# Performance work log

Hardware: AMD Instinct MI355X
Metric: run time of the kernel (lower is better)

## Reference

```python
import jax, jax.numpy as jnp
import numpy as np

N = 100000
E = 1600000
F_IN = 512
H1, C1 = 8, 8      # layer-1: 8 heads, 8 dims each (concat -> 64)
H2, C2 = 1, 16     # layer-2: 1 head, num_classes=16
SLOPE = 0.2        # GATConv leaky_relu negative slope


def setup_inputs() -> dict:
    key = jax.random.key(0)
    ks = jax.random.split(key, 10)
    x = jax.random.normal(ks[0], (N, F_IN), dtype=jnp.float32)
    edge_index = jax.random.randint(ks[1], (2, E), 0, N, dtype=jnp.int32)
    s = 0.05
    W1 = jax.random.normal(ks[2], (F_IN, H1 * C1), dtype=jnp.float32) * s
    a1_src = jax.random.normal(ks[3], (H1, C1), dtype=jnp.float32) * s
    a1_dst = jax.random.normal(ks[4], (H1, C1), dtype=jnp.float32) * s
    b1 = jnp.zeros((H1 * C1,), dtype=jnp.float32)
    W2 = jax.random.normal(ks[5], (H1 * C1, H2 * C2), dtype=jnp.float32) * s
    a2_src = jax.random.normal(ks[6], (H2, C2), dtype=jnp.float32) * s
    a2_dst = jax.random.normal(ks[7], (H2, C2), dtype=jnp.float32) * s
    b2 = jnp.zeros((H2 * C2,), dtype=jnp.float32)
    return {"x": x, "edge_index": edge_index, "W1": W1, "a1_src": a1_src,
            "a1_dst": a1_dst, "b1": b1, "W2": W2, "a2_src": a2_src,
            "a2_dst": a2_dst, "b2": b2}


def _gat_conv(h, src, dst, W, a_src, a_dst, b, heads, ch):
    n = h.shape[0]
    hp = (h @ W).reshape(n, heads, ch)                      # [N,H,C]
    al_s = jnp.einsum('nhc,hc->nh', hp, a_src)              # [N,H]
    al_d = jnp.einsum('nhc,hc->nh', hp, a_dst)              # [N,H]
    e = jax.nn.leaky_relu(al_s[src] + al_d[dst], SLOPE)     # [E,H]
    # segment softmax over edges sharing a destination (self-loops guarantee >=1 edge/node)
    emax = jax.lax.stop_gradient(jax.ops.segment_max(e, dst, num_segments=n))
    ee = jnp.exp(e - emax[dst])
    denom = jax.ops.segment_sum(ee, dst, num_segments=n)
    alpha = ee / denom[dst]                                 # [E,H]
    msg = hp[src] * alpha[:, :, None]                       # [E,H,C]
    out = jax.ops.segment_sum(msg, dst, num_segments=n)     # [N,H,C]
    return out.reshape(n, heads * ch) + b


def reference(x, edge_index, W1, a1_src, a1_dst, b1, W2, a2_src, a2_dst, b2):
    n = x.shape[0]
    loops = jnp.arange(n, dtype=edge_index.dtype)           # add_self_loops=True
    src = jnp.concatenate([edge_index[0], loops])
    dst = jnp.concatenate([edge_index[1], loops])
    h = jax.nn.elu(_gat_conv(x, src, dst, W1, a1_src, a1_dst, b1, H1, C1))
    h = _gat_conv(h, src, dst, W2, a2_src, a2_dst, b2, H2, C2)
    return jax.nn.log_softmax(h, axis=1)
```

## Files before the change

kernel.cpp:

```cpp
#include <hip/hip_runtime.h>
#include <hip/hip_bf16.h>

#define N_NODES 100000
#define F_IN    512
#define H1      8
#define C1      8
#define D1      64
#define C2      16
#define SLOPE   0.2f
#define CAP     48
#define PSHIFT  9
#define PPART   196
#define CAPP    9216
#define CHUNK   4096

typedef __bf16 bf16_t;
typedef bf16_t bf16x8 __attribute__((ext_vector_type(8)));
typedef float  f32x4  __attribute__((ext_vector_type(4)));

__global__ __launch_bounds__(256) void part_kernel(
    const float* __restrict__ W1, bf16_t* __restrict__ W1b,
    const int* __restrict__ ei, int* __restrict__ pcnt, int2* __restrict__ pfifo,
    int E, int total)
{
    __shared__ int hist[PPART];
    __shared__ int lofs[PPART];
    __shared__ int gbase[PPART];
    __shared__ int cursor[PPART];
    __shared__ int sdata[256];
    __shared__ int2 fifo[CHUNK];

    const int t = threadIdx.x;
    const int chunk0 = (int)blockIdx.x * CHUNK;

    for (int i = (int)blockIdx.x * 256 + t; i < 64 * 512; i += (int)gridDim.x * 256) {
        int nn = i >> 9, k = i & 511;
        W1b[i] = (bf16_t)W1[k * 64 + nn];
    }

    for (int i = t; i < PPART; i += 256) hist[i] = 0;
    __syncthreads();

    int srcs[16], dsts[16];
    const int e0 = chunk0 + t * 16;
    if (e0 + 16 <= E) {
#pragma unroll
        for (int q = 0; q < 4; ++q) {
            int4 s = *(const int4*)(ei + e0 + q * 4);
            int4 d = *(const int4*)(ei + E + e0 + q * 4);
            srcs[q*4+0]=s.x; srcs[q*4+1]=s.y; srcs[q*4+2]=s.z; srcs[q*4+3]=s.w;
            dsts[q*4+0]=d.x; dsts[q*4+1]=d.y; dsts[q*4+2]=d.z; dsts[q*4+3]=d.w;
        }
    } else {
#pragma unroll
        for (int j = 0; j < 16; ++j) {
            int e = e0 + j;
            if (e < E)          { srcs[j] = ei[e]; dsts[j] = ei[E + e]; }
            else if (e < total) { srcs[j] = dsts[j] = e - E; }
            else                { srcs[j] = -1;    dsts[j] = -1; }
        }
    }
#pragma unroll
    for (int j = 0; j < 16; ++j)
        if (dsts[j] >= 0) atomicAdd(&hist[dsts[j] >> PSHIFT], 1);
    __syncthreads();

    int hv = (t < PPART) ? hist[t] : 0;
    sdata[t] = hv;
    __syncthreads();
    for (int off = 1; off < 256; off <<= 1) {
        int x = (t >= off) ? sdata[t - off] : 0;
        __syncthreads();
        sdata[t] += x;
        __syncthreads();
    }
    if (t < PPART) {
        int lo = sdata[t] - hv;
        lofs[t]   = lo;
        cursor[t] = lo;
        gbase[t]  = hv ? atomicAdd(&pcnt[t], hv) : 0;
    }
    __syncthreads();

#pragma unroll
    for (int j = 0; j < 16; ++j) {
        if (dsts[j] >= 0) {
            int p = dsts[j] >> PSHIFT;
            int slot = atomicAdd(&cursor[p], 1);
            fifo[slot] = make_int2(srcs[j], dsts[j]);
        }
    }
    __syncthreads();

    const int w = t >> 6, lane = t & 63;
    for (int p = w; p < PPART; p += 4) {
        int len = hist[p];
        int lo  = lofs[p];
        int gb  = gbase[p];
        int2* dstp = pfifo + (size_t)p * CAPP;
        for (int j = lane; j < len; j += 64) {
            int g = gb + j;
            if (g < CAPP) dstp[g] = fifo[lo + j];
        }
    }
}

__global__ __launch_bounds__(512, 4) void pg_kernel(
    const int2* __restrict__ pfifo, const int* __restrict__ pcnt,
    int* __restrict__ buckets, int* __restrict__ cnt,
    const float* __restrict__ X, const bf16_t* __restrict__ Bt,
    const float* __restrict__ a1s, const float* __restrict__ a1d,
    bf16_t* __restrict__ HPb, float* __restrict__ als1, float* __restrict__ ald1,
    int n)
{
    __shared__ int lcnt[1 << PSHIFT];
    __shared__ __align__(16) bf16_t Bsm[8 * 4 * 64 * 8];

    const int t = threadIdx.x;

    if (blockIdx.x < PPART) {
        const int p = blockIdx.x;
        const int dbase = p << PSHIFT;
        const int nd = min(1 << PSHIFT, n - dbase);
        for (int i = t; i < nd; i += 512) lcnt[i] = 0;
        __syncthreads();

        int len = pcnt[p]; if (len > CAPP) len = CAPP;
        const int2* f = pfifo + (size_t)p * CAPP;

        int i = t;
        for (; i + 1536 < len; i += 2048) {
            int2 e0 = f[i], e1 = f[i + 512], e2 = f[i + 1024], e3 = f[i + 1536];
            int s0 = atomicAdd(&lcnt[e0.y - dbase], 1);
            int s1 = atomicAdd(&lcnt[e1.y - dbase], 1);
            int s2 = atomicAdd(&lcnt[e2.y - dbase], 1);
            int s3 = atomicAdd(&lcnt[e3.y - dbase], 1);
            if (s0 < CAP) buckets[(size_t)e0.y * CAP + s0] = e0.x;
            if (s1 < CAP) buckets[(size_t)e1.y * CAP + s1] = e1.x;
            if (s2 < CAP) buckets[(size_t)e2.y * CAP + s2] = e2.x;
            if (s3 < CAP) buckets[(size_t)e3.y * CAP + s3] = e3.x;
        }
        for (; i < len; i += 512) {
            int2 e = f[i];
            int s = atomicAdd(&lcnt[e.y - dbase], 1);
            if (s < CAP) buckets[(size_t)e.y * CAP + s] = e.x;
        }
        __syncthreads();
        for (int i2 = t; i2 < nd; i2 += 512) cnt[dbase + i2] = min(lcnt[i2], CAP);
        return;
    }

    const int rowbase = ((int)blockIdx.x - PPART) * 128;
    const int w = t >> 6;
    const int lane = t & 63;

    const int rloc = lane & 15;
    const int koff = (lane >> 4) * 8;

    int grow = rowbase + w * 16 + rloc;
    int growc = (grow < n) ? grow : (n - 1);
    const float* arow = X + (size_t)growc * F_IN + koff;

    f32x4 acc[4];
#pragma unroll
    for (int nt = 0; nt < 4; ++nt) acc[nt] = (f32x4){0.f, 0.f, 0.f, 0.f};

#pragma unroll
    for (int half = 0; half < 2; ++half) {
        for (int i = t; i < 2048; i += 512) {
            int l9 = i & 63;
            int nt = (i >> 6) & 3;
            int ks = i >> 8;
            int row = nt * 16 + (l9 & 15);
            int col = (half * 8 + ks) * 32 + (l9 >> 4) * 8;
            *(bf16x8*)(Bsm + (size_t)i * 8) =
                *(const bf16x8*)(Bt + (size_t)row * F_IN + col);
        }
        __syncthreads();

#pragma unroll 4
        for (int ks = 0; ks < 8; ++ks) {
            int kg = (half * 8 + ks) * 32;
            float4 xa0 = *(const float4*)(arow + kg);
            float4 xa1 = *(const float4*)(arow + kg + 4);
            bf16x8 af;
            af[0]=(bf16_t)xa0.x; af[1]=(bf16_t)xa0.y; af[2]=(bf16_t)xa0.z; af[3]=(bf16_t)xa0.w;
            af[4]=(bf16_t)xa1.x; af[5]=(bf16_t)xa1.y; af[6]=(bf16_t)xa1.z; af[7]=(bf16_t)xa1.w;
#pragma unroll
            for (int nt = 0; nt < 4; ++nt) {
                bf16x8 b = *(const bf16x8*)(Bsm + ((ks * 4 + nt) * 64 + lane) * 8);
                acc[nt] = __builtin_amdgcn_mfma_f32_16x16x32_bf16(af, b, acc[nt], 0, 0, 0);
            }
        }
        __syncthreads();
    }

    const int colg = lane & 15;
    const int quad = lane >> 4;
    const int b    = colg >> 3;
    float cs[4], cd[4];
#pragma unroll
    for (int nt = 0; nt < 4; ++nt) {
        cs[nt] = a1s[nt * 16 + colg];
        cd[nt] = a1d[nt * 16 + colg];
    }

#pragma unroll
    for (int i = 0; i < 4; ++i) {
        int r = rowbase + w * 16 + quad * 4 + i;
        bool ok = r < n;
        if (ok) {
            bf16_t* hr = HPb + (size_t)r * D1;
            hr[colg]      = (bf16_t)acc[0][i];
            hr[16 + colg] = (bf16_t)acc[1][i];
            hr[32 + colg] = (bf16_t)acc[2][i];
            hr[48 + colg] = (bf16_t)acc[3][i];
        }
#pragma unroll
        for (int nt = 0; nt < 4; ++nt) {
            float ps = acc[nt][i] * cs[nt];
            float pd = acc[nt][i] * cd[nt];
            ps += __shfl_xor(ps, 1, 64);  pd += __shfl_xor(pd, 1, 64);
            ps += __shfl_xor(ps, 2, 64);  pd += __shfl_xor(pd, 2, 64);
            ps += __shfl_xor(ps, 4, 64);  pd += __shfl_xor(pd, 4, 64);
            if (ok && (colg & 7) == 0) {
                als1[(size_t)r * 8 + 2 * nt + b] = ps;
                ald1[(size_t)r * 8 + 2 * nt + b] = pd;
            }
        }
    }
}

#define AGG1_SEC(G0)                                                        \
    {                                                                       \
        _Pragma("unroll")                                                   \
        for (int j = G0; j < G0 + 16; ++j) {                                \
            int s = bp[j];                                                  \
            s = (j < m) ? s : 0;           \
            float wgt = wbuf[wv][h][j];                                     \
            float v = (float)hp1[(size_t)s * D1 + lane];                    \
            acc = fmaf(wgt, v, acc);                                        \
        }                                                                   \
    }

__global__ __launch_bounds__(256, 2) void agg1_kernel(
    const bf16_t* __restrict__ hp1,
    const float* __restrict__ als, const float* __restrict__ ald,
    const int* __restrict__ cnt, const int* __restrict__ buckets,
    const float* __restrict__ b1,
    const float* __restrict__ W2,
    const float* __restrict__ a2s, const float* __restrict__ a2d,
    bf16_t* __restrict__ HP2b, float* __restrict__ als2, float* __restrict__ ald2,
    int n)
{
    __shared__ float Wsm[64 * 17];
    __shared__ float wbuf[4][8][50];

    const int t = threadIdx.x;
    for (int i = t; i < 1024; i += 256)
        Wsm[(i >> 4) * 17 + (i & 15)] = W2[i];
    __syncthreads();

    const int wv = t >> 6;
    const int lane = t & 63;
    int node = blockIdx.x * 4 + wv;
    if (node >= n) return;
    node = __builtin_amdgcn_readfirstlane(node);
    const int h = lane >> 3;

    int m = cnt[node]; if (m > CAP) m = CAP;
    m = __builtin_amdgcn_readfirstlane(m);
    const int* bp = buckets + (size_t)node * CAP;
    float ad = ald[node * 8 + h];

    const int jbase = lane & 7;
    float wsum = 0.f;
#pragma unroll
    for (int r = 0; r < 6; ++r) {
        int j = jbase + 8 * r;
        int s = (j < m) ? bp[j] : 0;
        float e = als[s * 8 + h] + ad;
        e = (e > 0.f) ? e : SLOPE * e;
        float wgt = (j < m) ? __expf(e) : 0.f;
        wbuf[wv][h][j] = wgt;
        wsum += wgt;
    }
    wsum += __shfl_xor(wsum, 1, 64);
    wsum += __shfl_xor(wsum, 2, 64);
    wsum += __shfl_xor(wsum, 4, 64);
    const float den = wsum;

    float acc = 0.f;
    AGG1_SEC(0);
    if (m > 16) AGG1_SEC(16);
    if (m > 32) AGG1_SEC(32);

    float v = acc / den + b1[lane];
    v = (v > 0.f) ? v : (__expf(v) - 1.f);

    const int g2 = lane >> 4, c = lane & 15;
    float o = 0.f;
#pragma unroll
    for (int kk = 0; kk < 16; ++kk) {
        float hk = __shfl(v, g2 * 16 + kk, 64);
        o = fmaf(hk, Wsm[(g2 * 16 + kk) * 17 + c], o);
    }
    o += __shfl_xor(o, 16, 64);
    o += __shfl_xor(o, 32, 64);
    if (g2 == 0) HP2b[(size_t)node * 16 + c] = (bf16_t)o;

    float rs = o * a2s[c];
    float rd = o * a2d[c];
    rs += __shfl_xor(rs, 1, 64);  rd += __shfl_xor(rd, 1, 64);
    rs += __shfl_xor(rs, 2, 64);  rd += __shfl_xor(rd, 2, 64);
    rs += __shfl_xor(rs, 4, 64);  rd += __shfl_xor(rd, 4, 64);
    rs += __shfl_xor(rs, 8, 64);  rd += __shfl_xor(rd, 8, 64);
    if (lane == 0) { als2[node] = rs; ald2[node] = rd; }
}

#define AGG2_SEC(G0)                                                        \
    {                                                                       \
        _Pragma("unroll")                                                   \
        for (int j = G0; j < G0 + 16; ++j) {                                \
            int s = bp[j];                                                  \
            s = (j < m) ? s : 0;                                            \
            float wgt = wbuf[nib][j];                                       \
            float v = (float)hp2[(size_t)s * 16 + c];                       \
            acc = fmaf(wgt, v, acc);                                        \
        }                                                                   \
    }

__global__ __launch_bounds__(256, 2) void agg2_kernel(
    const bf16_t* __restrict__ hp2,
    const float* __restrict__ als, const float* __restrict__ ald,
    const int* __restrict__ cnt, const int* __restrict__ buckets,
    const float* __restrict__ b2,
    float* __restrict__ out, int n)
{
    __shared__ float wbuf[16][50];
    const int t = threadIdx.x;
    const int nib = t >> 4;
    int node = blockIdx.x * 16 + nib;
    if (node >= n) return;
    const int c = t & 15;

    int m = cnt[node]; if (m > CAP) m = CAP;
    const int* bp = buckets + (size_t)node * CAP;
    float ad = ald[node];

    float wsum = 0.f;
#pragma unroll
    for (int r = 0; r < 3; ++r) {
        int j = c + 16 * r;
        int s = (j < m) ? bp[j] : 0;
        float e = als[s] + ad;
        e = (e > 0.f) ? e : SLOPE * e;
        float wgt = (j < m) ? __expf(e) : 0.f;
        wbuf[nib][j] = wgt;
        wsum += wgt;
    }
    wsum += __shfl_xor(wsum, 1, 16);
    wsum += __shfl_xor(wsum, 2, 16);
    wsum += __shfl_xor(wsum, 4, 16);
    wsum += __shfl_xor(wsum, 8, 16);
    const float den = wsum;

    float acc = 0.f;
    AGG2_SEC(0);
    if (m > 16) AGG2_SEC(16);
    if (m > 32) AGG2_SEC(32);

    float v = acc / den + b2[c];

    float mx = v;
    mx = fmaxf(mx, __shfl_xor(mx, 8, 16));
    mx = fmaxf(mx, __shfl_xor(mx, 4, 16));
    mx = fmaxf(mx, __shfl_xor(mx, 2, 16));
    mx = fmaxf(mx, __shfl_xor(mx, 1, 16));
    float ex = __expf(v - mx);
    float sum = ex;
    sum += __shfl_xor(sum, 8, 16);
    sum += __shfl_xor(sum, 4, 16);
    sum += __shfl_xor(sum, 2, 16);
    sum += __shfl_xor(sum, 1, 16);
    out[(size_t)node * 16 + c] = v - mx - __logf(sum);
}

extern "C" void kernel_launch(void* const* d_in, const int* in_sizes, int n_in,
                              void* d_out, int out_size, void* d_ws, size_t ws_size,
                              hipStream_t stream)
{
    const float* x      = (const float*)d_in[0];
    const int*   ei     = (const int*)  d_in[1];
    const float* W1     = (const float*)d_in[2];
    const float* a1_src = (const float*)d_in[3];
    const float* a1_dst = (const float*)d_in[4];
    const float* b1     = (const float*)d_in[5];
    const float* W2     = (const float*)d_in[6];
    const float* a2_src = (const float*)d_in[7];
    const float* a2_dst = (const float*)d_in[8];
    const float* b2     = (const float*)d_in[9];
    float* out = (float*)d_out;

    const int N = in_sizes[0] / F_IN;
    const int E = in_sizes[1] / 2;
    const int TOT = E + N;

    char* base = (char*)d_ws;
    size_t off = 0;
    auto carve = [&](size_t bytes) -> char* {
        char* p = base + off;
        off += (bytes + 255) & ~(size_t)255;
        return p;
    };
    bf16_t* hp1b    = (bf16_t*)carve((size_t)N * D1 * 2);
    float*  h1      = (float*) carve((size_t)N * D1 * 4);
    bf16_t* hp2b    = (bf16_t*)carve((size_t)N * 16 * 2);
    float*  als1    = (float*) carve((size_t)N * 8 * 4);
    float*  ald1    = (float*) carve((size_t)N * 8 * 4);
    float*  als2    = (float*) carve((size_t)N * 4);
    float*  ald2    = (float*) carve((size_t)N * 4);
    int*    cnt     = (int*)   carve((size_t)N * 4);
    int*    pcnt    = (int*)   carve((size_t)PPART * 4);
    int*    buckets = (int*)   carve((size_t)N * CAP * 4);
    bf16_t* W1b     = (bf16_t*)carve((size_t)64 * 512 * 2);
    int2*  pfifo   = (int2*)h1;

    const int Gp = (TOT + CHUNK - 1) / CHUNK;
    const int Gg = (N + 127) / 128;

    hipMemsetAsync(pcnt, 0, (size_t)PPART * 4, stream);

    part_kernel<<<Gp, 256, 0, stream>>>(W1, W1b, ei, pcnt, pfifo, E, TOT);

    pg_kernel<<<PPART + Gg, 512, 0, stream>>>(pfifo, pcnt, buckets, cnt,
                                              x, W1b, a1_src, a1_dst,
                                              hp1b, als1, ald1, N);

    agg1_kernel<<<(N + 3) / 4, 256, 0, stream>>>(hp1b, als1, ald1, cnt, buckets,
                                                 b1, W2, a2_src, a2_dst,
                                                 hp2b, als2, ald2, N);

    agg2_kernel<<<(N + 15) / 16, 256, 0, stream>>>(hp2b, als2, ald2, cnt, buckets, b2, out, N);
}
```

Before: 468.2 us.

## Overlap edge partitioning with layer-1 GEMM and split bucket placement kernel

Moves the edge-partition pass into the GEMM launch so the partition blocks run alongside the projection blocks, with shared memory held in a union. Bucket placement becomes its own kernel after that launch, and the W1 bf16 conversion gets a small kernel of its own. Partitions shrink to 256 nodes with smaller chunks, which gives more blocks and less per-block shared memory. The aggregation loops now step in groups of 8 rather than 16 to skip padded neighbours, at the cost of more branches and one extra launch.

```diff
diff --git a/kernel.cpp b/kernel.cpp
--- a/kernel.cpp
+++ b/kernel.cpp
@@ -9,148 +9,112 @@
 #define C2      16
 #define SLOPE   0.2f
 #define CAP     48
-#define PSHIFT  9
-#define PPART   196
-#define CAPP    9216
-#define CHUNK   4096
+#define PSHIFT  8
+#define PPART   391
+#define CAPP    5120
+#define CHUNK   2048
 
 typedef __bf16 bf16_t;
 typedef bf16_t bf16x8 __attribute__((ext_vector_type(8)));
 typedef float  f32x4  __attribute__((ext_vector_type(4)));
 
-__global__ __launch_bounds__(256) void part_kernel(
-    const float* __restrict__ W1, bf16_t* __restrict__ W1b,
+__global__ __launch_bounds__(256) void wcvt_kernel(
+    const float* __restrict__ W, bf16_t* __restrict__ Bt)
+{
+    int i = blockIdx.x * 256 + threadIdx.x;
+    if (i >= 64 * 512) return;
+    int nn = i >> 9, k = i & 511;
+    Bt[i] = (bf16_t)W[k * 64 + nn];
+}
+
+union PgSmem {
+    struct {
+        int hist[PPART], lofs[PPART], gbase[PPART], cursor[PPART];
+        int sdata[512];
+        int2 fifo[CHUNK];
+    } part;
+    bf16_t Bsm[8 * 4 * 64 * 8];
+};
+
+__global__ __launch_bounds__(512, 4) void pg_kernel(
     const int* __restrict__ ei, int* __restrict__ pcnt, int2* __restrict__ pfifo,
-    int E, int total)
-{
-    __shared__ int hist[PPART];
-    __shared__ int lofs[PPART];
-    __shared__ int gbase[PPART];
-    __shared__ int cursor[PPART];
-    __shared__ int sdata[256];
-    __shared__ int2 fifo[CHUNK];
-
-    const int t = threadIdx.x;
-    const int chunk0 = (int)blockIdx.x * CHUNK;
-
-    for (int i = (int)blockIdx.x * 256 + t; i < 64 * 512; i += (int)gridDim.x * 256) {
-        int nn = i >> 9, k = i & 511;
-        W1b[i] = (bf16_t)W1[k * 64 + nn];
-    }
-
-    for (int i = t; i < PPART; i += 256) hist[i] = 0;
-    __syncthreads();
-
-    int srcs[16], dsts[16];
-    const int e0 = chunk0 + t * 16;
-    if (e0 + 16 <= E) {
-#pragma unroll
-        for (int q = 0; q < 4; ++q) {
-            int4 s = *(const int4*)(ei + e0 + q * 4);
-            int4 d = *(const int4*)(ei + E + e0 + q * 4);
-            srcs[q*4+0]=s.x; srcs[q*4+1]=s.y; srcs[q*4+2]=s.z; srcs[q*4+3]=s.w;
-            dsts[q*4+0]=d.x; dsts[q*4+1]=d.y; dsts[q*4+2]=d.z; dsts[q*4+3]=d.w;
-        }
-    } else {
-#pragma unroll
-        for (int j = 0; j < 16; ++j) {
-            int e = e0 + j;
-            if (e < E)          { srcs[j] = ei[e]; dsts[j] = ei[E + e]; }
-            else if (e < total) { srcs[j] = dsts[j] = e - E; }
-            else                { srcs[j] = -1;    dsts[j] = -1; }
-        }
-    }
-#pragma unroll
-    for (int j = 0; j < 16; ++j)
-        if (dsts[j] >= 0) atomicAdd(&hist[dsts[j] >> PSHIFT], 1);
-    __syncthreads();
-
-    int hv = (t < PPART) ? hist[t] : 0;
-    sdata[t] = hv;
-    __syncthreads();
-    for (int off = 1; off < 256; off <<= 1) {
-        int x = (t >= off) ? sdata[t - off] : 0;
-        __syncthreads();
-        sdata[t] += x;
-        __syncthreads();
-    }
-    if (t < PPART) {
-        int lo = sdata[t] - hv;
-        lofs[t]   = lo;
-        cursor[t] = lo;
-        gbase[t]  = hv ? atomicAdd(&pcnt[t], hv) : 0;
-    }
-    __syncthreads();
-
-#pragma unroll
-    for (int j = 0; j < 16; ++j) {
-        if (dsts[j] >= 0) {
-            int p = dsts[j] >> PSHIFT;
-            int slot = atomicAdd(&cursor[p], 1);
-            fifo[slot] = make_int2(srcs[j], dsts[j]);
-        }
-    }
-    __syncthreads();
-
-    const int w = t >> 6, lane = t & 63;
-    for (int p = w; p < PPART; p += 4) {
-        int len = hist[p];
-        int lo  = lofs[p];
-        int gb  = gbase[p];
-        int2* dstp = pfifo + (size_t)p * CAPP;
-        for (int j = lane; j < len; j += 64) {
-            int g = gb + j;
-            if (g < CAPP) dstp[g] = fifo[lo + j];
-        }
-    }
-}
-
-__global__ __launch_bounds__(512, 4) void pg_kernel(
-    const int2* __restrict__ pfifo, const int* __restrict__ pcnt,
-    int* __restrict__ buckets, int* __restrict__ cnt,
     const float* __restrict__ X, const bf16_t* __restrict__ Bt,
     const float* __restrict__ a1s, const float* __restrict__ a1d,
     bf16_t* __restrict__ HPb, float* __restrict__ als1, float* __restrict__ ald1,
-    int n)
-{
-    __shared__ int lcnt[1 << PSHIFT];
-    __shared__ __align__(16) bf16_t Bsm[8 * 4 * 64 * 8];
-
+    int E, int total, int Gg, int n)
+{
+    __shared__ PgSmem sm;
     const int t = threadIdx.x;
 
-    if (blockIdx.x < PPART) {
-        const int p = blockIdx.x;
-        const int dbase = p << PSHIFT;
-        const int nd = min(1 << PSHIFT, n - dbase);
-        for (int i = t; i < nd; i += 512) lcnt[i] = 0;
-        __syncthreads();
-
-        int len = pcnt[p]; if (len > CAPP) len = CAPP;
-        const int2* f = pfifo + (size_t)p * CAPP;
-
-        int i = t;
-        for (; i + 1536 < len; i += 2048) {
-            int2 e0 = f[i], e1 = f[i + 512], e2 = f[i + 1024], e3 = f[i + 1536];
-            int s0 = atomicAdd(&lcnt[e0.y - dbase], 1);
-            int s1 = atomicAdd(&lcnt[e1.y - dbase], 1);
-            int s2 = atomicAdd(&lcnt[e2.y - dbase], 1);
-            int s3 = atomicAdd(&lcnt[e3.y - dbase], 1);
-            if (s0 < CAP) buckets[(size_t)e0.y * CAP + s0] = e0.x;
-            if (s1 < CAP) buckets[(size_t)e1.y * CAP + s1] = e1.x;
-            if (s2 < CAP) buckets[(size_t)e2.y * CAP + s2] = e2.x;
-            if (s3 < CAP) buckets[(size_t)e3.y * CAP + s3] = e3.x;
-        }
-        for (; i < len; i += 512) {
-            int2 e = f[i];
-            int s = atomicAdd(&lcnt[e.y - dbase], 1);
-            if (s < CAP) buckets[(size_t)e.y * CAP + s] = e.x;
-        }
-        __syncthreads();
-        for (int i2 = t; i2 < nd; i2 += 512) cnt[dbase + i2] = min(lcnt[i2], CAP);
+    if ((int)blockIdx.x >= Gg) {
+        const int chunk0 = ((int)blockIdx.x - Gg) * CHUNK;
+
+        for (int i = t; i < PPART; i += 512) sm.part.hist[i] = 0;
+        __syncthreads();
+
+        int srcs[4], dsts[4];
+        const int e0 = chunk0 + t * 4;
+        if (e0 + 4 <= E) {
+            int4 s = *(const int4*)(ei + e0);
+            int4 d = *(const int4*)(ei + E + e0);
+            srcs[0]=s.x; srcs[1]=s.y; srcs[2]=s.z; srcs[3]=s.w;
+            dsts[0]=d.x; dsts[1]=d.y; dsts[2]=d.z; dsts[3]=d.w;
+        } else {
+#pragma unroll
+            for (int j = 0; j < 4; ++j) {
+                int e = e0 + j;
+                if (e < E)          { srcs[j] = ei[e]; dsts[j] = ei[E + e]; }
+                else if (e < total) { srcs[j] = dsts[j] = e - E; }
+                else                { srcs[j] = -1;    dsts[j] = -1; }
+            }
+        }
+#pragma unroll
+        for (int j = 0; j < 4; ++j)
+            if (dsts[j] >= 0) atomicAdd(&sm.part.hist[dsts[j] >> PSHIFT], 1);
+        __syncthreads();
+
+        int hv = (t < PPART) ? sm.part.hist[t] : 0;
+        sm.part.sdata[t] = hv;
+        __syncthreads();
+        for (int off = 1; off < 512; off <<= 1) {
+            int x = (t >= off) ? sm.part.sdata[t - off] : 0;
+            __syncthreads();
+            sm.part.sdata[t] += x;
+            __syncthreads();
+        }
+        if (t < PPART) {
+            int lo = sm.part.sdata[t] - hv;
+            sm.part.lofs[t]   = lo;
+            sm.part.cursor[t] = lo;
+            sm.part.gbase[t]  = hv ? atomicAdd(&pcnt[t], hv) : 0;
+        }
+        __syncthreads();
+
+#pragma unroll
+        for (int j = 0; j < 4; ++j) {
+            if (dsts[j] >= 0) {
+                int p = dsts[j] >> PSHIFT;
+                int slot = atomicAdd(&sm.part.cursor[p], 1);
+                sm.part.fifo[slot] = make_int2(srcs[j], dsts[j]);
+            }
+        }
+        __syncthreads();
+
+        const int w = t >> 6, lane = t & 63;
+        for (int p = w; p < PPART; p += 8) {
+            int len = sm.part.hist[p];
+            int lo  = sm.part.lofs[p];
+            int gb  = sm.part.gbase[p];
+            int2* dstp = pfifo + (size_t)p * CAPP;
+            for (int j = lane; j < len; j += 64) {
+                int g = gb + j;
+                if (g < CAPP) dstp[g] = sm.part.fifo[lo + j];
+            }
+        }
         return;
     }
 
-    const int rowbase = ((int)blockIdx.x - PPART) * 128;
+    const int rowbase = (int)blockIdx.x * 128;
     const int w = t >> 6;
     const int lane = t & 63;
 
@@ -173,7 +137,7 @@
             int ks = i >> 8;
             int row = nt * 16 + (l9 & 15);
             int col = (half * 8 + ks) * 32 + (l9 >> 4) * 8;
-            *(bf16x8*)(Bsm + (size_t)i * 8) =
+            *(bf16x8*)(sm.Bsm + (size_t)i * 8) =
                 *(const bf16x8*)(Bt + (size_t)row * F_IN + col);
         }
         __syncthreads();
@@ -188,7 +152,7 @@
             af[4]=(bf16_t)xa1.x; af[5]=(bf16_t)xa1.y; af[6]=(bf16_t)xa1.z; af[7]=(bf16_t)xa1.w;
 #pragma unroll
             for (int nt = 0; nt < 4; ++nt) {
-                bf16x8 b = *(const bf16x8*)(Bsm + ((ks * 4 + nt) * 64 + lane) * 8);
+                bf16x8 b = *(const bf16x8*)(sm.Bsm + ((ks * 4 + nt) * 64 + lane) * 8);
                 acc[nt] = __builtin_amdgcn_mfma_f32_16x16x32_bf16(af, b, acc[nt], 0, 0, 0);
             }
         }
@@ -231,10 +195,46 @@
     }
 }
 
+__global__ __launch_bounds__(512) void place_kernel(
+    const int2* __restrict__ pfifo, const int* __restrict__ pcnt,
+    int* __restrict__ buckets, int* __restrict__ cnt, int n)
+{
+    __shared__ int lcnt[1 << PSHIFT];
+    const int p = blockIdx.x;
+    const int dbase = p << PSHIFT;
+    const int nd = min(1 << PSHIFT, n - dbase);
+    const int t = threadIdx.x;
+    for (int i = t; i < nd; i += 512) lcnt[i] = 0;
+    __syncthreads();
+
+    int len = pcnt[p]; if (len > CAPP) len = CAPP;
+    const int2* f = pfifo + (size_t)p * CAPP;
+
+    int i = t;
+    for (; i + 1536 < len; i += 2048) {
+        int2 e0 = f[i], e1 = f[i + 512], e2 = f[i + 1024], e3 = f[i + 1536];
+        int s0 = atomicAdd(&lcnt[e0.y - dbase], 1);
+        int s1 = atomicAdd(&lcnt[e1.y - dbase], 1);
+        int s2 = atomicAdd(&lcnt[e2.y - dbase], 1);
+        int s3 = atomicAdd(&lcnt[e3.y - dbase], 1);
+        if (s0 < CAP) buckets[(size_t)e0.y * CAP + s0] = e0.x;
+        if (s1 < CAP) buckets[(size_t)e1.y * CAP + s1] = e1.x;
+        if (s2 < CAP) buckets[(size_t)e2.y * CAP + s2] = e2.x;
+        if (s3 < CAP) buckets[(size_t)e3.y * CAP + s3] = e3.x;
+    }
+    for (; i < len; i += 512) {
+        int2 e = f[i];
+        int s = atomicAdd(&lcnt[e.y - dbase], 1);
+        if (s < CAP) buckets[(size_t)e.y * CAP + s] = e.x;
+    }
+    __syncthreads();
+    for (int i2 = t; i2 < nd; i2 += 512) cnt[dbase + i2] = min(lcnt[i2], CAP);
+}
+
 #define AGG1_SEC(G0)                                                        \
     {                                                                       \
         _Pragma("unroll")                                                   \
-        for (int j = G0; j < G0 + 16; ++j) {                                \
+        for (int j = G0; j < G0 + 8; ++j) {                                 \
             int s = bp[j];                                                  \
             s = (j < m) ? s : 0;           \
             float wgt = wbuf[wv][h][j];                                     \
@@ -292,8 +292,11 @@
 
     float acc = 0.f;
     AGG1_SEC(0);
+    if (m > 8)  AGG1_SEC(8);
     if (m > 16) AGG1_SEC(16);
+    if (m > 24) AGG1_SEC(24);
     if (m > 32) AGG1_SEC(32);
+    if (m > 40) AGG1_SEC(40);
 
     float v = acc / den + b1[lane];
     v = (v > 0.f) ? v : (__expf(v) - 1.f);
@@ -321,7 +324,7 @@
 #define AGG2_SEC(G0)                                                        \
     {                                                                       \
         _Pragma("unroll")                                                   \
-        for (int j = G0; j < G0 + 16; ++j) {                                \
+        for (int j = G0; j < G0 + 8; ++j) {                                 \
             int s = bp[j];                                                  \
             s = (j < m) ? s : 0;                                            \
             float wgt = wbuf[nib][j];                                       \
@@ -367,8 +370,11 @@
 
     float acc = 0.f;
     AGG2_SEC(0);
+    if (m > 8)  AGG2_SEC(8);
     if (m > 16) AGG2_SEC(16);
+    if (m > 24) AGG2_SEC(24);
     if (m > 32) AGG2_SEC(32);
+    if (m > 40) AGG2_SEC(40);
 
     float v = acc / den + b2[c];
 
@@ -431,11 +437,14 @@
 
     hipMemsetAsync(pcnt, 0, (size_t)PPART * 4, stream);
 
-    part_kernel<<<Gp, 256, 0, stream>>>(W1, W1b, ei, pcnt, pfifo, E, TOT);
-
-    pg_kernel<<<PPART + Gg, 512, 0, stream>>>(pfifo, pcnt, buckets, cnt,
-                                              x, W1b, a1_src, a1_dst,
-                                              hp1b, als1, ald1, N);
+    wcvt_kernel<<<128, 256, 0, stream>>>(W1, W1b);
+
+    pg_kernel<<<Gg + Gp, 512, 0, stream>>>(ei, pcnt, pfifo,
+                                           x, W1b, a1_src, a1_dst,
+                                           hp1b, als1, ald1,
+                                           E, TOT, Gg, N);
+
+    place_kernel<<<PPART, 512, 0, stream>>>(pfifo, pcnt, buckets, cnt, N);
 
     agg1_kernel<<<(N + 3) / 4, 256, 0, stream>>>(hp1b, als1, ald1, cnt, buckets,
                                                  b1, W2, a2_src, a2_dst,
```

New measurement: 464.8 us. Within noise of the previous version (-0.7%).
